# Kernel tuning notes

Hardware: AMD Instinct MI355X
Metric: run time of the kernel (lower is better)

Reference implementation:

```python
import jax, jax.numpy as jnp
import numpy as np

B, D, H, L = 16384, 512, 1024, 2


def _lstm_step_zero_state(x, W_ih, W_hh, b_ih, b_hh):
    """One PyTorch-convention LSTM cell step with h0=c0=0.

    Gate order: i, f, g, o. With h0=0 the W_hh matmul contributes nothing,
    but both biases still apply (matches cuDNN/PyTorch math exactly).
    With c0=0 the forget-gate term f*c0 vanishes.
    x: (B, in), W_ih: (4H, in), W_hh: (4H, H), biases: (4H,)
    """
    gates = x @ W_ih.T + (b_ih + b_hh)  # (B, 4H)
    i, f, g, o = jnp.split(gates, 4, axis=-1)
    i = jax.nn.sigmoid(i)
    g = jnp.tanh(g)
    o = jax.nn.sigmoid(o)
    c = i * g  # f * c0 == 0
    h = o * jnp.tanh(c)
    return h


def setup_inputs() -> dict:
    key = jax.random.key(0)
    ks = jax.random.split(key, 12)
    s = 1.0 / np.sqrt(H)  # PyTorch LSTM init scale

    def u(k, shape):
        return jax.random.uniform(k, shape, jnp.float32, -s, s)

    x = jax.random.normal(ks[0], (B, D), jnp.float32)
    return {
        "x": x,
        "W_ih0": u(ks[1], (4 * H, D)),
        "W_hh0": u(ks[2], (4 * H, H)),
        "b_ih0": u(ks[3], (4 * H,)),
        "b_hh0": u(ks[4], (4 * H,)),
        "W_ih1": u(ks[5], (4 * H, H)),
        "W_hh1": u(ks[6], (4 * H, H)),
        "b_ih1": u(ks[7], (4 * H,)),
        "b_hh1": u(ks[8], (4 * H,)),
        "W_dec": u(ks[9], (D, H)),
        "b_dec": u(ks[10], (D,)),
    }


def reference(x, W_ih0, W_hh0, b_ih0, b_hh0, W_ih1, W_hh1, b_ih1, b_hh1, W_dec, b_dec):
    # forward(): x.unsqueeze(1) -> 2-layer LSTM (zero init state, 1 step) -> decoder
    h0 = _lstm_step_zero_state(x, W_ih0, W_hh0, b_ih0, b_hh0)   # (B, H)
    h1 = _lstm_step_zero_state(h0, W_ih1, W_hh1, b_ih1, b_hh1)  # (B, H)
    return h1 @ W_dec.T + b_dec  # (B, D)
```

## Files before the change

### kernel.cpp

```cpp
#include <hip/hip_runtime.h>
#include <stdint.h>


typedef __attribute__((ext_vector_type(8))) __bf16 bf16x8;
typedef __attribute__((ext_vector_type(4))) float f32x4;

#define BM 128
#define BK 64

__device__ __forceinline__ unsigned short f2b(float f) {
    unsigned int x = __builtin_bit_cast(unsigned int, f);
    x = x + 0x7FFFu + ((x >> 16) & 1u);
    return (unsigned short)(x >> 16);
}
__device__ __forceinline__ float sigf(float x) { return 1.0f / (1.0f + __expf(-x)); }
__device__ __forceinline__ float tanh_safe(float x) {
    float a = fabsf(x);
    float e = __expf(-2.0f * a);
    float t = (1.0f - e) / (1.0f + e);
    return x < 0.0f ? -t : t;
}

__device__ __forceinline__ void cvt8(const float* __restrict__ s,
                                     unsigned short* __restrict__ d) {
    f32x4 lo = *reinterpret_cast<const f32x4*>(s);
    f32x4 hi = *reinterpret_cast<const f32x4*>(s + 4);
    __attribute__((ext_vector_type(8))) unsigned short v;
    v[0] = f2b(lo[0]); v[1] = f2b(lo[1]); v[2] = f2b(lo[2]); v[3] = f2b(lo[3]);
    v[4] = f2b(hi[0]); v[5] = f2b(hi[1]); v[6] = f2b(hi[2]); v[7] = f2b(hi[3]);
    *reinterpret_cast<__attribute__((ext_vector_type(8))) unsigned short*>(d) = v;
}

__device__ __forceinline__ void gload16(const unsigned short* g, unsigned short* l) {
    __builtin_amdgcn_global_load_lds(
        (const __attribute__((address_space(1))) void*)g,
        (__attribute__((address_space(3))) void*)l,
        16, 0, 0);
}

__global__ __launch_bounds__(256) void cvt_lin(const float* __restrict__ s,
                                               unsigned short* __restrict__ d,
                                               int n8) {
    int stride = gridDim.x * blockDim.x;
    for (int c = blockIdx.x * blockDim.x + threadIdx.x; c < n8; c += stride)
        cvt8(s + (size_t)c * 8, d + (size_t)c * 8);
}

__global__ __launch_bounds__(256) void pack_w(const float* __restrict__ W,
                                              unsigned short* __restrict__ d,
                                              int K8, int H, int n8) {
    int stride = gridDim.x * blockDim.x;
    for (int c = blockIdx.x * blockDim.x + threadIdx.x; c < n8; c += stride) {
        int dstRow = c / K8, kc = c - dstRow * K8;
        int G = dstRow / 192, r = dstRow - G * 192;
        int wc = r / 96, rr = r - wc * 96;
        int n = rr >> 4, i = rr & 15;
        int hsub = n / 3, gate = n - hsub * 3;
        int goff = (gate == 0) ? 0 : (gate + 1);
        int hcol = G * 64 + wc * 32 + hsub * 16 + i;
        cvt8(W + ((size_t)(goff * H + hcol) * K8 + kc) * 8, d + (size_t)c * 8);
    }
}

template <int GATED>
__global__ __launch_bounds__(256, 3) void gemm_fused(
    const unsigned short* __restrict__ A,
    const unsigned short* __restrict__ Wp,
    const float* __restrict__ b0,
    const float* __restrict__ b1,
    void* __restrict__ Ov,
    int M, int K, int N, int NBX)
{
    constexpr int NFR   = GATED ? 6 : 4;
    constexpr int BROWS = GATED ? 192 : 128;
    constexpr int WCS   = GATED ? 96 : 64;
    constexpr int ONB   = GATED ? 64 : 128;
    constexpr int NBCH  = BROWS / 32;

    __shared__ __align__(16) unsigned short sA[BM * BK];
    __shared__ __align__(16) unsigned short sB[BROWS * BK];

    const int tid  = threadIdx.x;
    const int lane = tid & 63;
    const int w    = tid >> 6;
    const int wr   = w >> 1, wc = w & 1;
    const int l16  = lane & 15, hi8 = lane >> 4;

    const int cpx  = gridDim.x >> 3;
    const int orig = blockIdx.x;
    const int rid  = (orig & 7) * cpx + (orig >> 3);
    const int bx   = rid % NBX;
    const int by   = rid / NBX;
    const int row0 = by * BM;
    const int n0   = bx * ONB;

    const int r0 = tid >> 3, sl = tid & 7;
    const int ls = sl ^ (r0 & 7);
    const unsigned int strd = 32u * (unsigned)K;
    unsigned int offA = (unsigned)(row0 + r0) * (unsigned)K + ls * 8;
    unsigned int offB = (unsigned)(GATED ? bx * BROWS + r0 : n0 + r0)
                        * (unsigned)K + ls * 8;

    f32x4 acc[4][NFR];
#pragma unroll
    for (int m = 0; m < 4; ++m)
#pragma unroll
        for (int n = 0; n < NFR; ++n)
            acc[m][n] = (f32x4){0.f, 0.f, 0.f, 0.f};

    for (int k0 = 0; k0 < K; k0 += BK) {
#pragma unroll
        for (int i = 0; i < 4; ++i)
            gload16(A + offA + i * strd + k0, sA + tid * 8 + i * 2048);
#pragma unroll
        for (int i = 0; i < NBCH; ++i)
            gload16(Wp + offB + i * strd + k0, sB + tid * 8 + i * 2048);
        __syncthreads();

#pragma unroll
        for (int ks = 0; ks < 2; ++ks) {
            bf16x8 av[4], bv[NFR];
#pragma unroll
            for (int m = 0; m < 4; ++m) {
                int row = wr * 64 + m * 16 + l16;
                int ps = (ks * 4 + hi8) ^ (row & 7);
                av[m] = *reinterpret_cast<const bf16x8*>(sA + row * BK + ps * 8);
            }
#pragma unroll
            for (int n = 0; n < NFR; ++n) {
                int row = wc * WCS + n * 16 + l16;
                int ps = (ks * 4 + hi8) ^ (row & 7);
                bv[n] = *reinterpret_cast<const bf16x8*>(sB + row * BK + ps * 8);
            }
#pragma unroll
            for (int m = 0; m < 4; ++m)
#pragma unroll
                for (int n = 0; n < NFR; ++n)
                    acc[m][n] = __builtin_amdgcn_mfma_f32_16x16x32_bf16(
                        av[m], bv[n], acc[m][n], 0, 0, 0);
        }
        __syncthreads();
    }

    if constexpr (GATED) {
        unsigned short* O = (unsigned short*)Ov;
#pragma unroll
        for (int hsub = 0; hsub < 2; ++hsub) {
            const int hcol = n0 + wc * 32 + hsub * 16 + l16;
            const float bi = b0[hcol]         + b1[hcol];
            const float bg = b0[2 * N + hcol] + b1[2 * N + hcol];
            const float bo = b0[3 * N + hcol] + b1[3 * N + hcol];
#pragma unroll
            for (int m = 0; m < 4; ++m) {
                int rbase = row0 + wr * 64 + m * 16 + hi8 * 4;
#pragma unroll
                for (int q = 0; q < 4; ++q) {
                    float iv = sigf(acc[m][hsub * 3 + 0][q] + bi);
                    float gv = tanh_safe(acc[m][hsub * 3 + 1][q] + bg);
                    float ov = sigf(acc[m][hsub * 3 + 2][q] + bo);
                    float h  = ov * tanh_safe(iv * gv);
                    O[(size_t)(rbase + q) * N + hcol] = f2b(h);
                }
            }
        }
    } else {
        float* O = (float*)Ov;
#pragma unroll
        for (int n = 0; n < NFR; ++n) {
            int col = n0 + wc * WCS + n * 16 + l16;
            float bias = b0[col];
#pragma unroll
            for (int m = 0; m < 4; ++m) {
                int rbase = row0 + wr * 64 + m * 16 + hi8 * 4;
#pragma unroll
                for (int q = 0; q < 4; ++q)
                    O[(size_t)(rbase + q) * N + col] = acc[m][n][q] + bias;
            }
        }
    }
}

extern "C" void kernel_launch(void* const* d_in, const int* in_sizes, int n_in,
                              void* d_out, int out_size, void* d_ws, size_t ws_size,
                              hipStream_t stream) {
    constexpr int M = 16384, D = 512, H = 1024;

    const float* x    = (const float*)d_in[0];
    const float* Wih0 = (const float*)d_in[1];
    const float* bih0 = (const float*)d_in[3];
    const float* bhh0 = (const float*)d_in[4];
    const float* Wih1 = (const float*)d_in[5];
    const float* bih1 = (const float*)d_in[7];
    const float* bhh1 = (const float*)d_in[8];
    const float* Wdec = (const float*)d_in[9];
    const float* bdec = (const float*)d_in[10];

    const size_t szH = (size_t)M * H * 2;
    const size_t sw0 = (size_t)3 * H * D * 2;
    const size_t sw1 = (size_t)3 * H * H * 2;

    unsigned short* h0 = (unsigned short*)d_ws;
    unsigned short* h1 = (unsigned short*)((char*)d_ws + szH);
    unsigned short* xb = h1;
    unsigned short* wp0   = (unsigned short*)((char*)d_ws + 2 * szH);
    unsigned short* wp1   = (unsigned short*)((char*)wp0 + sw0);
    unsigned short* wdecb = (unsigned short*)((char*)wp1 + sw1);

    cvt_lin<<<2048, 256, 0, stream>>>(x, xb, M * D / 8);
    pack_w <<<768,  256, 0, stream>>>(Wih0, wp0, D / 8, H, 3 * H * D / 8);
    pack_w <<<1536, 256, 0, stream>>>(Wih1, wp1, H / 8, H, 3 * H * H / 8);
    cvt_lin<<<256,  256, 0, stream>>>(Wdec, wdecb, D * H / 8);

    gemm_fused<1><<<dim3((H / 64) * (M / BM)), 256, 0, stream>>>(
        xb, wp0, bih0, bhh0, h0, M, D, H, H / 64);
    gemm_fused<1><<<dim3((H / 64) * (M / BM)), 256, 0, stream>>>(
        h0, wp1, bih1, bhh1, h1, M, H, H, H / 64);
    gemm_fused<0><<<dim3((D / 128) * (M / BM)), 256, 0, stream>>>(
        h1, wdecb, bdec, nullptr, (float*)d_out, M, H, D, D / 128);
}
```

Measured before the change: 215.6 us.

## Double-buffer LDS tiles with interleaved async prefetch and MFMA scheduling

Turns the GEMM main loop into a double-buffered pipeline. Global-to-LDS loads for the next K tile are split into chunks and interleaved between MFMA groups, with explicit vmcnt/lgkmcnt waits, sched barriers and setprio around the MFMA groups. K and N become template constants so the address math compiles to constants. LDS use doubles and the occupancy hint drops from 3 to 2 blocks per CU, trading occupancy for latency hiding within each block.

```diff
diff --git a/kernel.cpp b/kernel.cpp
--- a/kernel.cpp
+++ b/kernel.cpp
@@ -37,6 +37,11 @@
         (__attribute__((address_space(3))) void*)l,
         16, 0, 0);
 }
+
+#define VMW(n)  asm volatile("s_waitcnt vmcnt(" #n ")" ::: "memory")
+#define LGKM0() asm volatile("s_waitcnt lgkmcnt(0)" ::: "memory")
+#define SB0()   __builtin_amdgcn_sched_barrier(0)
+#define BAR()   __builtin_amdgcn_s_barrier()
 
 __global__ __launch_bounds__(256) void cvt_lin(const float* __restrict__ s,
                                                unsigned short* __restrict__ d,
@@ -62,23 +67,28 @@
     }
 }
 
-template <int GATED>
-__global__ __launch_bounds__(256, 3) void gemm_fused(
+template <int GATED, int K, int N>
+__global__ __launch_bounds__(256, 2) void gemm_fused(
     const unsigned short* __restrict__ A,
     const unsigned short* __restrict__ Wp,
     const float* __restrict__ b0,
     const float* __restrict__ b1,
     void* __restrict__ Ov,
-    int M, int K, int N, int NBX)
+    int M)
 {
     constexpr int NFR   = GATED ? 6 : 4;
     constexpr int BROWS = GATED ? 192 : 128;
     constexpr int WCS   = GATED ? 96 : 64;
     constexpr int ONB   = GATED ? 64 : 128;
-    constexpr int NBCH  = BROWS / 32;
-
-    __shared__ __align__(16) unsigned short sA[BM * BK];
-    __shared__ __align__(16) unsigned short sB[BROWS * BK];
+    constexpr int NBX   = N / ONB;
+    constexpr int ACH   = 4;
+    constexpr int BCH   = BROWS / 32;
+    constexpr int AE    = BM * BK;
+    constexpr int BE    = BROWS * BK;
+    constexpr int NT    = K / BK;
+
+    __shared__ __align__(16) unsigned short sA[2 * AE];
+    __shared__ __align__(16) unsigned short sB[2 * BE];
 
     const int tid  = threadIdx.x;
     const int lane = tid & 63;
@@ -96,10 +106,30 @@
 
     const int r0 = tid >> 3, sl = tid & 7;
     const int ls = sl ^ (r0 & 7);
-    const unsigned int strd = 32u * (unsigned)K;
-    unsigned int offA = (unsigned)(row0 + r0) * (unsigned)K + ls * 8;
-    unsigned int offB = (unsigned)(GATED ? bx * BROWS + r0 : n0 + r0)
-                        * (unsigned)K + ls * 8;
+    const unsigned int offA = (unsigned)(row0 + r0) * K + ls * 8;
+    const unsigned int offB = (unsigned)((GATED ? bx * BROWS : n0) + r0) * K + ls * 8;
+
+#define STG(u, nbuf, koff)                                                     \
+    do {                                                                       \
+        if ((u) < ACH)                                                         \
+            gload16(A + offA + (u) * (32 * K) + (koff),                        \
+                    sA + (nbuf) * AE + tid * 8 + (u) * 2048);                  \
+        else                                                                   \
+            gload16(Wp + offB + ((u) - ACH) * (32 * K) + (koff),               \
+                    sB + (nbuf) * BE + tid * 8 + ((u) - ACH) * 2048);          \
+    } while (0)
+
+    bf16x8 av[4];
+#define LDAV(ks, b_)                                                           \
+    do {                                                                       \
+        _Pragma("unroll")                                                      \
+        for (int m = 0; m < 4; ++m) {                                          \
+            int row = wr * 64 + m * 16 + l16;                                  \
+            int ps = ((ks) * 4 + hi8) ^ (row & 7);                             \
+            av[m] = *reinterpret_cast<const bf16x8*>(                          \
+                sA + (b_) * AE + row * BK + ps * 8);                           \
+        }                                                                      \
+    } while (0)
 
     f32x4 acc[4][NFR];
 #pragma unroll
@@ -108,41 +138,62 @@
         for (int n = 0; n < NFR; ++n)
             acc[m][n] = (f32x4){0.f, 0.f, 0.f, 0.f};
 
-    for (int k0 = 0; k0 < K; k0 += BK) {
-#pragma unroll
-        for (int i = 0; i < 4; ++i)
-            gload16(A + offA + i * strd + k0, sA + tid * 8 + i * 2048);
-#pragma unroll
-        for (int i = 0; i < NBCH; ++i)
-            gload16(Wp + offB + i * strd + k0, sB + tid * 8 + i * 2048);
-        __syncthreads();
-
-#pragma unroll
-        for (int ks = 0; ks < 2; ++ks) {
-            bf16x8 av[4], bv[NFR];
-#pragma unroll
-            for (int m = 0; m < 4; ++m) {
-                int row = wr * 64 + m * 16 + l16;
-                int ps = (ks * 4 + hi8) ^ (row & 7);
-                av[m] = *reinterpret_cast<const bf16x8*>(sA + row * BK + ps * 8);
-            }
-#pragma unroll
-            for (int n = 0; n < NFR; ++n) {
-                int row = wc * WCS + n * 16 + l16;
-                int ps = (ks * 4 + hi8) ^ (row & 7);
-                bv[n] = *reinterpret_cast<const bf16x8*>(sB + row * BK + ps * 8);
-            }
-#pragma unroll
-            for (int m = 0; m < 4; ++m)
-#pragma unroll
-                for (int n = 0; n < NFR; ++n)
-                    acc[m][n] = __builtin_amdgcn_mfma_f32_16x16x32_bf16(
-                        av[m], bv[n], acc[m][n], 0, 0, 0);
+#pragma unroll
+    for (int u = 0; u < ACH + BCH; ++u) STG(u, 0, 0);
+
+    if constexpr (GATED) {
+        bf16x8 bv[3];
+#define LDBV3(ks, nh, b_)                                                      \
+    do {                                                                       \
+        _Pragma("unroll")                                                      \
+        for (int j = 0; j < 3; ++j) {                                          \
+            int row = wc * WCS + ((nh) * 3 + j) * 16 + l16;                    \
+            int ps = ((ks) * 4 + hi8) ^ (row & 7);                             \
+            bv[j] = *reinterpret_cast<const bf16x8*>(                          \
+                sB + (b_) * BE + row * BK + ps * 8);                           \
+        }                                                                      \
+    } while (0)
+#define MMG(nh)                                                                \
+    do {                                                                       \
+        __builtin_amdgcn_s_setprio(1);                                         \
+        _Pragma("unroll")                                                      \
+        for (int m = 0; m < 4; ++m) {                                          \
+            _Pragma("unroll")                                                  \
+            for (int j = 0; j < 3; ++j)                                        \
+                acc[m][(nh) * 3 + j] = __builtin_amdgcn_mfma_f32_16x16x32_bf16(\
+                    av[m], bv[j], acc[m][(nh) * 3 + j], 0, 0, 0);              \
+        }                                                                      \
+        __builtin_amdgcn_s_setprio(0);                                         \
+    } while (0)
+
+        for (int t = 0; t < NT; ++t) {
+            const int b = t & 1, nb = b ^ 1;
+            const int ko = (t + 1) * BK;
+            const bool st = (t + 1 < NT);
+            if (st) { STG(0, nb, ko); STG(1, nb, ko); STG(2, nb, ko); VMW(3); }
+            else    { VMW(0); }
+            BAR(); SB0();
+            LDAV(0, b); LDBV3(0, 0, b);
+            LGKM0(); SB0();
+            MMG(0);
+            BAR();
+            LDBV3(0, 1, b);
+            if (st) { STG(3, nb, ko); STG(4, nb, ko); STG(5, nb, ko); }
+            BAR(); LGKM0(); SB0();
+            MMG(1);
+            BAR();
+            LDAV(1, b); LDBV3(1, 0, b);
+            if (st) { STG(6, nb, ko); STG(7, nb, ko); }
+            BAR(); LGKM0(); SB0();
+            MMG(0);
+            BAR();
+            LDBV3(1, 1, b);
+            if (st) { STG(8, nb, ko); STG(9, nb, ko); }
+            BAR(); LGKM0(); SB0();
+            MMG(1);
+            BAR();
         }
-        __syncthreads();
-    }
-
-    if constexpr (GATED) {
+
         unsigned short* O = (unsigned short*)Ov;
 #pragma unroll
         for (int hsub = 0; hsub < 2; ++hsub) {
@@ -164,9 +215,51 @@
             }
         }
     } else {
+        bf16x8 bv[4];
+#define LDBV4(ks, b_)                                                          \
+    do {                                                                       \
+        _Pragma("unroll")                                                      \
+        for (int j = 0; j < 4; ++j) {                                          \
+            int row = wc * WCS + j * 16 + l16;                                 \
+            int ps = ((ks) * 4 + hi8) ^ (row & 7);                             \
+            bv[j] = *reinterpret_cast<const bf16x8*>(                          \
+                sB + (b_) * BE + row * BK + ps * 8);                           \
+        }                                                                      \
+    } while (0)
+#define MMD()                                                                  \
+    do {                                                                       \
+        __builtin_amdgcn_s_setprio(1);                                         \
+        _Pragma("unroll")                                                      \
+        for (int m = 0; m < 4; ++m) {                                          \
+            _Pragma("unroll")                                                  \
+            for (int j = 0; j < 4; ++j)                                        \
+                acc[m][j] = __builtin_amdgcn_mfma_f32_16x16x32_bf16(           \
+                    av[m], bv[j], acc[m][j], 0, 0, 0);                         \
+        }                                                                      \
+        __builtin_amdgcn_s_setprio(0);                                         \
+    } while (0)
+
+        for (int t = 0; t < NT; ++t) {
+            const int b = t & 1, nb = b ^ 1;
+            const int ko = (t + 1) * BK;
+            const bool st = (t + 1 < NT);
+            if (st) { STG(0, nb, ko); STG(1, nb, ko); STG(2, nb, ko); STG(3, nb, ko); VMW(4); }
+            else    { VMW(0); }
+            BAR(); SB0();
+            LDAV(0, b); LDBV4(0, b);
+            LGKM0(); SB0();
+            MMD();
+            BAR();
+            LDAV(1, b); LDBV4(1, b);
+            if (st) { STG(4, nb, ko); STG(5, nb, ko); STG(6, nb, ko); STG(7, nb, ko); }
+            BAR(); LGKM0(); SB0();
+            MMD();
+            BAR();
+        }
+
         float* O = (float*)Ov;
 #pragma unroll
-        for (int n = 0; n < NFR; ++n) {
+        for (int n = 0; n < 4; ++n) {
             int col = n0 + wc * WCS + n * 16 + l16;
             float bias = b0[col];
 #pragma unroll
@@ -178,6 +271,12 @@
             }
         }
     }
+#undef STG
+#undef LDAV
+#undef LDBV3
+#undef MMG
+#undef LDBV4
+#undef MMD
 }
 
 extern "C" void kernel_launch(void* const* d_in, const int* in_sizes, int n_in,
@@ -211,10 +310,10 @@
     pack_w <<<1536, 256, 0, stream>>>(Wih1, wp1, H / 8, H, 3 * H * H / 8);
     cvt_lin<<<256,  256, 0, stream>>>(Wdec, wdecb, D * H / 8);
 
-    gemm_fused<1><<<dim3((H / 64) * (M / BM)), 256, 0, stream>>>(
-        xb, wp0, bih0, bhh0, h0, M, D, H, H / 64);
-    gemm_fused<1><<<dim3((H / 64) * (M / BM)), 256, 0, stream>>>(
-        h0, wp1, bih1, bhh1, h1, M, H, H, H / 64);
-    gemm_fused<0><<<dim3((D / 128) * (M / BM)), 256, 0, stream>>>(
-        h1, wdecb, bdec, nullptr, (float*)d_out, M, H, D, D / 128);
-}
+    gemm_fused<1, 512, 1024><<<dim3((1024 / 64) * (M / BM)), 256, 0, stream>>>(
+        xb, wp0, bih0, bhh0, h0, M);
+    gemm_fused<1, 1024, 1024><<<dim3((1024 / 64) * (M / BM)), 256, 0, stream>>>(
+        h0, wp1, bih1, bhh1, h1, M);
+    gemm_fused<0, 1024, 512><<<dim3((512 / 128) * (M / BM)), 256, 0, stream>>>(
+        h1, wdecb, bdec, nullptr, (float*)d_out, M);
+}
```

New measurement: 245.0 us. 1.14x slower.

## Double-buffer LDS tiles to overlap global loads with MFMA compute

Applied to the files above, without the earlier changes.

Doubles the shared-memory A and B tiles and prefetches the next K tile into the alternate buffer while the current tile is being multiplied. One barrier per iteration replaces two, and global latency can hide behind the MFMA work. Occupancy drops from 3 to 2 blocks per CU because of the larger LDS footprint and the changed launch bounds.

```diff
diff --git a/kernel.cpp b/kernel.cpp
--- a/kernel.cpp
+++ b/kernel.cpp
@@ -63,7 +63,7 @@
 }
 
 template <int GATED>
-__global__ __launch_bounds__(256, 3) void gemm_fused(
+__global__ __launch_bounds__(256, 2) void gemm_fused(
     const unsigned short* __restrict__ A,
     const unsigned short* __restrict__ Wp,
     const float* __restrict__ b0,
@@ -76,9 +76,11 @@
     constexpr int WCS   = GATED ? 96 : 64;
     constexpr int ONB   = GATED ? 64 : 128;
     constexpr int NBCH  = BROWS / 32;
-
-    __shared__ __align__(16) unsigned short sA[BM * BK];
-    __shared__ __align__(16) unsigned short sB[BROWS * BK];
+    constexpr int AE    = BM * BK;
+    constexpr int BE    = BROWS * BK;
+
+    __shared__ __align__(16) unsigned short sA[2 * AE];
+    __shared__ __align__(16) unsigned short sB[2 * BE];
 
     const int tid  = threadIdx.x;
     const int lane = tid & 63;
@@ -97,9 +99,9 @@
     const int r0 = tid >> 3, sl = tid & 7;
     const int ls = sl ^ (r0 & 7);
     const unsigned int strd = 32u * (unsigned)K;
-    unsigned int offA = (unsigned)(row0 + r0) * (unsigned)K + ls * 8;
-    unsigned int offB = (unsigned)(GATED ? bx * BROWS + r0 : n0 + r0)
-                        * (unsigned)K + ls * 8;
+    const unsigned int offA = (unsigned)(row0 + r0) * (unsigned)K + ls * 8;
+    const unsigned int offB = (unsigned)((GATED ? bx * BROWS : n0) + r0)
+                              * (unsigned)K + ls * 8;
 
     f32x4 acc[4][NFR];
 #pragma unroll
@@ -108,15 +110,32 @@
         for (int n = 0; n < NFR; ++n)
             acc[m][n] = (f32x4){0.f, 0.f, 0.f, 0.f};
 
-    for (int k0 = 0; k0 < K; k0 += BK) {
-#pragma unroll
-        for (int i = 0; i < 4; ++i)
-            gload16(A + offA + i * strd + k0, sA + tid * 8 + i * 2048);
-#pragma unroll
-        for (int i = 0; i < NBCH; ++i)
-            gload16(Wp + offB + i * strd + k0, sB + tid * 8 + i * 2048);
-        __syncthreads();
-
+#pragma unroll
+    for (int i = 0; i < 4; ++i)
+        gload16(A + offA + i * strd, sA + tid * 8 + i * 2048);
+#pragma unroll
+    for (int i = 0; i < NBCH; ++i)
+        gload16(Wp + offB + i * strd, sB + tid * 8 + i * 2048);
+    __syncthreads();
+
+    const int NT = K >> 6;
+    for (int t = 0; t < NT; ++t) {
+        const int b = t & 1, nb = b ^ 1;
+
+        if (t + 1 < NT) {
+            const unsigned int kn = (unsigned)(t + 1) * BK;
+#pragma unroll
+            for (int i = 0; i < 4; ++i)
+                gload16(A + offA + i * strd + kn,
+                        sA + nb * AE + tid * 8 + i * 2048);
+#pragma unroll
+            for (int i = 0; i < NBCH; ++i)
+                gload16(Wp + offB + i * strd + kn,
+                        sB + nb * BE + tid * 8 + i * 2048);
+        }
+
+        const unsigned short* sAb = sA + b * AE;
+        const unsigned short* sBb = sB + b * BE;
 #pragma unroll
         for (int ks = 0; ks < 2; ++ks) {
             bf16x8 av[4], bv[NFR];
@@ -124,13 +143,13 @@
             for (int m = 0; m < 4; ++m) {
                 int row = wr * 64 + m * 16 + l16;
                 int ps = (ks * 4 + hi8) ^ (row & 7);
-                av[m] = *reinterpret_cast<const bf16x8*>(sA + row * BK + ps * 8);
+                av[m] = *reinterpret_cast<const bf16x8*>(sAb + row * BK + ps * 8);
             }
 #pragma unroll
             for (int n = 0; n < NFR; ++n) {
                 int row = wc * WCS + n * 16 + l16;
                 int ps = (ks * 4 + hi8) ^ (row & 7);
-                bv[n] = *reinterpret_cast<const bf16x8*>(sB + row * BK + ps * 8);
+                bv[n] = *reinterpret_cast<const bf16x8*>(sBb + row * BK + ps * 8);
             }
 #pragma unroll
             for (int m = 0; m < 4; ++m)
```

New measurement: 234.7 us. 1.09x slower.
